# Optimization experiments

Measured on AMD Instinct MI355X. Metric: run time of the kernel, lower is better.

## Reference

```python
import jax, jax.numpy as jnp
import numpy as np

EMB_SIZE = 768
NUM_HEADS = 8


def setup_inputs() -> dict:
    key = jax.random.key(0)
    ks = jax.random.split(key, 6)
    B, N, E = 8, 1024, EMB_SIZE
    return {
        "x": jax.random.normal(ks[0], (B, N, E), dtype=jnp.float32),
        "relative_pos": jax.random.normal(ks[1], (NUM_HEADS, N, N), dtype=jnp.float32),
        "qkv_w": jax.random.normal(ks[2], (2 * E, E), dtype=jnp.float32) * 0.02,
        "qkv_b": jax.random.normal(ks[3], (2 * E,), dtype=jnp.float32) * 0.02,
        "val_w": jax.random.normal(ks[4], (E, E), dtype=jnp.float32) * 0.02,
        "val_b": jax.random.normal(ks[5], (E,), dtype=jnp.float32) * 0.02,
    }


def reference(x, relative_pos, qkv_w, qkv_b, val_w, val_b):
    B, N, E = x.shape
    H = NUM_HEADS
    D = E // H
    # qkv projection: [B, N, 2E]; last dim layout is (h, d, qk) per einops rearrange
    qkv = (x @ qkv_w.T + qkv_b).reshape(B, N, H, D, 2)
    q = jnp.transpose(qkv[..., 0], (0, 2, 1, 3))  # [B, H, N, D]
    k = jnp.transpose(qkv[..., 1], (0, 2, 1, 3))  # [B, H, N, D]
    scale = E ** 0.5  # original divides by sqrt(emb_size), not sqrt(d_head)
    energy = jnp.einsum('bhqd,bhkd->bhqk', q, k) / scale  # [B, H, N, N]
    # relative_pos [H, N, N] broadcasts over batch
    energy = jax.nn.softmax(energy + relative_pos, axis=-1)
    values = x @ val_w.T + val_b  # [B, N, E]
    return values, energy
```

## Files before the change

kernel.cpp:

```cpp
#include <hip/hip_runtime.h>
#include <hip/hip_bf16.h>

#define EMB 768
#define NH 8
#define DH 96
#define BATCH 8
#define SEQ 1024
#define M_TOT (BATCH * SEQ)
#define NCOLS (3 * EMB)

typedef float f32x4 __attribute__((ext_vector_type(4)));
typedef __bf16 bf16x8 __attribute__((ext_vector_type(8)));

__device__ __forceinline__ unsigned short f2bf_bits(float f) {
  __hip_bfloat16 b = __float2bfloat16(f);
  return *reinterpret_cast<unsigned short*>(&b);
}

__device__ __forceinline__ void gload_lds16(const void* g, void* l) {
  __builtin_amdgcn_global_load_lds(
      (__attribute__((address_space(1))) void*)(g),
      (__attribute__((address_space(3))) void*)(l), 16, 0, 0);
}

__global__ void prep_x_kernel(const float* __restrict__ x, __hip_bfloat16* __restrict__ xb) {
  const int n4 = M_TOT * EMB / 4;
  int i = blockIdx.x * blockDim.x + threadIdx.x;
  if (i < n4) {
    f32x4 v = reinterpret_cast<const f32x4*>(x)[i];
    ushort4 o;
    o.x = f2bf_bits(v[0]);
    o.y = f2bf_bits(v[1]);
    o.z = f2bf_bits(v[2]);
    o.w = f2bf_bits(v[3]);
    reinterpret_cast<ushort4*>(xb)[i] = o;
  }
}

__global__ void prep_w_kernel(const float* __restrict__ qkv_w, const float* __restrict__ qkv_b,
                              const float* __restrict__ val_w, const float* __restrict__ val_b,
                              __hip_bfloat16* __restrict__ Wall, float* __restrict__ bias) {
  const float inv_s = 0.03608439182435161f;
  int idx = blockIdx.x * 256 + threadIdx.x;
  if (idx >= NCOLS * EMB) return;
  int r = idx / EMB;
  int c = idx - r * EMB;
  float v;
  if (r < EMB) {
    int h = r / DH, d = r - h * DH;
    int src = h * 192 + 2 * d;
    v = qkv_w[(size_t)src * EMB + c] * inv_s;
    if (c == 0) bias[r] = qkv_b[src] * inv_s;
  } else if (r < 2 * EMB) {
    int r2 = r - EMB;
    int h = r2 / DH, d = r2 - h * DH;
    int src = h * 192 + 2 * d + 1;
    v = qkv_w[(size_t)src * EMB + c];
    if (c == 0) bias[r] = qkv_b[src];
  } else {
    int r3 = r - 2 * EMB;
    v = val_w[(size_t)r3 * EMB + c];
    if (c == 0) bias[r] = val_b[r3];
  }
  Wall[idx] = __float2bfloat16(v);
}

__global__ __launch_bounds__(256) void gemm_kernel(
    const __hip_bfloat16* __restrict__ xb, const __hip_bfloat16* __restrict__ Wall,
    const float* __restrict__ bias, __hip_bfloat16* __restrict__ qhead,
    __hip_bfloat16* __restrict__ khead, float* __restrict__ vout) {
  __shared__ __hip_bfloat16 As[128 * 32];
  __shared__ __hip_bfloat16 Bs[128 * 32];
  __shared__ __hip_bfloat16 Cs[128][136];
  const int tid = threadIdx.x;
  const int w = tid >> 6, l = tid & 63;
  const int m0 = blockIdx.x * 128;
  const int n0 = blockIdx.y * 128;
  const int wr = w >> 1, wc = w & 1;

  f32x4 acc[4][4] = {};

  const int sr0 = (w * 2 + 0) * 16 + (l >> 2);
  const int sr1 = (w * 2 + 1) * 16 + (l >> 2);
  const int sc = (l & 3) * 8;

  for (int kt = 0; kt < EMB / 32; ++kt) {
    const int k0 = kt * 32;
    gload_lds16(xb + (size_t)(m0 + sr0) * EMB + k0 + sc, (void*)(As + (w * 2 + 0) * 512));
    gload_lds16(xb + (size_t)(m0 + sr1) * EMB + k0 + sc, (void*)(As + (w * 2 + 1) * 512));
    gload_lds16(Wall + (size_t)(n0 + sr0) * EMB + k0 + sc, (void*)(Bs + (w * 2 + 0) * 512));
    gload_lds16(Wall + (size_t)(n0 + sr1) * EMB + k0 + sc, (void*)(Bs + (w * 2 + 1) * 512));
    __syncthreads();

    bf16x8 af[4], bfr[4];
#pragma unroll
    for (int t = 0; t < 4; ++t) {
      af[t] = *reinterpret_cast<const bf16x8*>(As + (wr * 64 + t * 16 + (l & 15)) * 32 + (l >> 4) * 8);
      bfr[t] = *reinterpret_cast<const bf16x8*>(Bs + (wc * 64 + t * 16 + (l & 15)) * 32 + (l >> 4) * 8);
    }
#pragma unroll
    for (int i = 0; i < 4; ++i)
#pragma unroll
      for (int j = 0; j < 4; ++j)
        acc[i][j] = __builtin_amdgcn_mfma_f32_16x16x32_bf16(af[i], bfr[j], acc[i][j], 0, 0, 0);
    __syncthreads();
  }

  if (n0 >= 2 * EMB) {
    const int rowbase = m0 + wr * 64;
    const int colbase = n0 - 2 * EMB + wc * 64;
#pragma unroll
    for (int j = 0; j < 4; ++j) {
      const int n = colbase + j * 16 + (l & 15);
      const float bb = bias[2 * EMB + n];
#pragma unroll
      for (int i = 0; i < 4; ++i) {
#pragma unroll
        for (int q = 0; q < 4; ++q) {
          const int m = rowbase + i * 16 + (l >> 4) * 4 + q;
          vout[(size_t)m * EMB + n] = acc[i][j][q] + bb;
        }
      }
    }
  } else {
#pragma unroll
    for (int j = 0; j < 4; ++j) {
      const int nl = wc * 64 + j * 16 + (l & 15);
      const float bb = bias[n0 + nl];
#pragma unroll
      for (int i = 0; i < 4; ++i) {
#pragma unroll
        for (int q = 0; q < 4; ++q) {
          const int ml = wr * 64 + i * 16 + (l >> 4) * 4 + q;
          Cs[ml][nl] = __float2bfloat16(acc[i][j][q] + bb);
        }
      }
    }
    __syncthreads();
    __hip_bfloat16* dst = (n0 >= EMB) ? khead : qhead;
    const int ch0 = (n0 >= EMB) ? (n0 - EMB) : n0;
    const int cg = (tid & 15) * 8;
    const int gch = ch0 + cg;
    const int hh = gch / DH, dd = gch - hh * DH;
#pragma unroll
    for (int pass = 0; pass < 8; ++pass) {
      const int r = pass * 16 + (tid >> 4);
      const int m = m0 + r;
      const int bb_ = m >> 10, mm = m & 1023;
      bf16x8 v8 = *reinterpret_cast<const bf16x8*>(&Cs[r][cg]);
      *reinterpret_cast<bf16x8*>(dst + ((size_t)(bb_ * NH + hh) * SEQ + mm) * DH + dd) = v8;
    }
  }
}

__global__ __launch_bounds__(512, 2) void attn_kernel(
    const __hip_bfloat16* __restrict__ qhead, const __hip_bfloat16* __restrict__ khead,
    const float* __restrict__ rel, float* __restrict__ eout) {
  __shared__ alignas(16) char KS[8 * 3 * 3072];
  __shared__ float redm[16][8];
  __shared__ float reds[16][8];

  const int t = threadIdx.x;
  const int w = t >> 6, l = t & 63;
  const int lr = l >> 4, lc = l & 15;
  const int flat = blockIdx.x;
  const int u = flat >> 6;
  const int b = (flat >> 3) & 7;
  const int g = u * 8 + (flat & 7);
  const int h = g >> 6;
  const int rb = g & 63;
  const int row0 = rb * 16;

  const __hip_bfloat16* qsrc = qhead + ((size_t)(b * NH + h) * SEQ + row0 + lc) * DH;
  bf16x8 qf[3];
#pragma unroll
  for (int kc = 0; kc < 3; ++kc)
    qf[kc] = *reinterpret_cast<const bf16x8*>(qsrc + kc * 32 + lr * 8);

  const float* relsrc = rel + ((size_t)h * SEQ + row0 + lc) * SEQ + w * 16 + lr * 4;
  f32x4 relv[8];
#pragma unroll
  for (int c = 0; c < 8; ++c)
    relv[c] = *reinterpret_cast<const f32x4*>(relsrc + c * 128);

  const __hip_bfloat16* ksrc =
      khead + (size_t)(b * NH + h) * SEQ * DH + (size_t)w * 16 * DH;
  char* kdst = KS + w * 9216;

#define STAGE_K(c, buf)                                                             \
  {                                                                                 \
    const __hip_bfloat16* s_ = ksrc + (size_t)(c) * 12288 + (size_t)l * 8;          \
    gload_lds16(s_, kdst + (buf) * 3072);                                           \
    gload_lds16(s_ + 512, kdst + (buf) * 3072 + 1024);                              \
    gload_lds16(s_ + 1024, kdst + (buf) * 3072 + 2048);                             \
  }

  STAGE_K(0, 0)
  STAGE_K(1, 1)

  f32x4 acc[8];
#pragma unroll
  for (int c = 0; c < 8; ++c) {
    if (c < 6) STAGE_K(c + 2, (c + 2) % 3)
    if (c < 6) {
      asm volatile("s_waitcnt vmcnt(6)" ::: "memory");
    } else if (c == 6) {
      asm volatile("s_waitcnt vmcnt(3)" ::: "memory");
    } else {
      asm volatile("s_waitcnt vmcnt(0)" ::: "memory");
    }
    __builtin_amdgcn_sched_barrier(0);
    const __hip_bfloat16* kp =
        reinterpret_cast<const __hip_bfloat16*>(kdst + (c % 3) * 3072) + lc * DH;
    f32x4 a = {0.f, 0.f, 0.f, 0.f};
    __builtin_amdgcn_s_setprio(1);
#pragma unroll
    for (int kc = 0; kc < 3; ++kc) {
      bf16x8 kf = *reinterpret_cast<const bf16x8*>(kp + kc * 32 + lr * 8);
      a = __builtin_amdgcn_mfma_f32_16x16x32_bf16(kf, qf[kc], a, 0, 0, 0);
    }
    __builtin_amdgcn_s_setprio(0);
    acc[c] = a + relv[c];
  }
#undef STAGE_K

  float mx = -3.4e38f;
#pragma unroll
  for (int c = 0; c < 8; ++c)
    mx = fmaxf(mx, fmaxf(fmaxf(acc[c][0], acc[c][1]), fmaxf(acc[c][2], acc[c][3])));
  mx = fmaxf(mx, __shfl_xor(mx, 16));
  mx = fmaxf(mx, __shfl_xor(mx, 32));
  if (l < 16) redm[lc][w] = mx;
  __syncthreads();
  float M = redm[lc][0];
#pragma unroll
  for (int i = 1; i < 8; ++i) M = fmaxf(M, redm[lc][i]);

  float sm = 0.f;
#pragma unroll
  for (int c = 0; c < 8; ++c) {
#pragma unroll
    for (int j = 0; j < 4; ++j) {
      float e = __expf(acc[c][j] - M);
      acc[c][j] = e;
      sm += e;
    }
  }
  sm += __shfl_xor(sm, 16);
  sm += __shfl_xor(sm, 32);
  if (l < 16) reds[lc][w] = sm;
  __syncthreads();
  float S = 0.f;
#pragma unroll
  for (int i = 0; i < 8; ++i) S += reds[lc][i];
  const float rinv = 1.0f / S;

  float* op = eout + ((size_t)(b * NH + h) * SEQ + row0 + lc) * SEQ + w * 16 + lr * 4;
#pragma unroll
  for (int c = 0; c < 8; ++c) {
    f32x4 v = acc[c] * rinv;
    *reinterpret_cast<f32x4*>(op + c * 128) = v;
  }
}

extern "C" void kernel_launch(void* const* d_in, const int* in_sizes, int n_in,
                              void* d_out, int out_size, void* d_ws, size_t ws_size,
                              hipStream_t stream) {
  const float* x = (const float*)d_in[0];
  const float* rel = (const float*)d_in[1];
  const float* qkv_w = (const float*)d_in[2];
  const float* qkv_b = (const float*)d_in[3];
  const float* val_w = (const float*)d_in[4];
  const float* val_b = (const float*)d_in[5];
  float* out = (float*)d_out;

  char* ws = (char*)d_ws;
  __hip_bfloat16* xb = (__hip_bfloat16*)(ws);
  __hip_bfloat16* Wall = (__hip_bfloat16*)(ws + 12582912);
  float* bias = (float*)(ws + 16121856);
  __hip_bfloat16* qhead = (__hip_bfloat16*)(ws + 16131072);
  __hip_bfloat16* khead = (__hip_bfloat16*)(ws + 28713984);

  float* vout = out;
  float* eout = out + (size_t)M_TOT * EMB;

  prep_x_kernel<<<dim3(M_TOT * EMB / 4 / 256), dim3(256), 0, stream>>>(x, xb);
  prep_w_kernel<<<dim3(NCOLS * EMB / 256), dim3(256), 0, stream>>>(qkv_w, qkv_b, val_w, val_b,
                                                                   Wall, bias);
  gemm_kernel<<<dim3(M_TOT / 128, NCOLS / 128), dim3(256), 0, stream>>>(xb, Wall, bias, qhead,
                                                                        khead, vout);
  attn_kernel<<<dim3(SEQ / 16 * NH * BATCH), dim3(512), 0, stream>>>(qhead, khead, rel, eout);
}
```

Before: 182.4 us.

## Process 32 query rows per attention block with 16 waves and swizzled K LDS

Each attention block now handles 32 query rows, split into two 16-row MFMA tiles, using 1024 threads and 16 waves. Each K tile staged into LDS is reused for both query tiles, which halves K global traffic per output row. The K staging also applies an XOR swizzle on the LDS address to avoid bank conflicts on the fragment reads. The cost is more LDS and registers per block, which may lower occupancy; the launch bounds of (1024,4) also look aggressive.

```diff
diff --git a/kernel.cpp b/kernel.cpp
--- a/kernel.cpp
+++ b/kernel.cpp
@@ -153,12 +153,12 @@
   }
 }
 
-__global__ __launch_bounds__(512, 2) void attn_kernel(
+__global__ __launch_bounds__(1024, 4) void attn_kernel(
     const __hip_bfloat16* __restrict__ qhead, const __hip_bfloat16* __restrict__ khead,
     const float* __restrict__ rel, float* __restrict__ eout) {
-  __shared__ alignas(16) char KS[8 * 3 * 3072];
-  __shared__ float redm[16][8];
-  __shared__ float reds[16][8];
+  __shared__ alignas(16) char KS[16 * 3 * 3072];
+  __shared__ float redm[32][16];
+  __shared__ float reds[32][16];
 
   const int t = threadIdx.x;
   const int w = t >> 6, l = t & 63;
@@ -167,99 +167,148 @@
   const int u = flat >> 6;
   const int b = (flat >> 3) & 7;
   const int g = u * 8 + (flat & 7);
-  const int h = g >> 6;
-  const int rb = g & 63;
-  const int row0 = rb * 16;
-
-  const __hip_bfloat16* qsrc = qhead + ((size_t)(b * NH + h) * SEQ + row0 + lc) * DH;
-  bf16x8 qf[3];
-#pragma unroll
-  for (int kc = 0; kc < 3; ++kc)
-    qf[kc] = *reinterpret_cast<const bf16x8*>(qsrc + kc * 32 + lr * 8);
-
-  const float* relsrc = rel + ((size_t)h * SEQ + row0 + lc) * SEQ + w * 16 + lr * 4;
-  f32x4 relv[8];
-#pragma unroll
-  for (int c = 0; c < 8; ++c)
-    relv[c] = *reinterpret_cast<const f32x4*>(relsrc + c * 128);
-
-  const __hip_bfloat16* ksrc =
-      khead + (size_t)(b * NH + h) * SEQ * DH + (size_t)w * 16 * DH;
+  const int h = g >> 5;
+  const int rb = g & 31;
+  const int row0 = rb * 32;
+  const size_t bh = (size_t)(b * NH + h);
+
+  const __hip_bfloat16* qbase = qhead + (bh * SEQ + row0 + lc) * DH;
+  bf16x8 qf[2][3];
+#pragma unroll
+  for (int tt = 0; tt < 2; ++tt)
+#pragma unroll
+    for (int kc = 0; kc < 3; ++kc)
+      qf[tt][kc] = *reinterpret_cast<const bf16x8*>(qbase + (size_t)(tt * 16) * DH + kc * 32 + lr * 8);
+
+  const float* relbase = rel + ((size_t)h * SEQ + row0 + lc) * SEQ + w * 16 + lr * 4;
+  f32x4 relv[4][2];
+#pragma unroll
+  for (int c = 0; c < 4; ++c)
+#pragma unroll
+    for (int tt = 0; tt < 2; ++tt)
+      relv[c][tt] = *reinterpret_cast<const f32x4*>(relbase + (size_t)(tt * 16) * SEQ + c * 256);
+
+  const __hip_bfloat16* kbh = khead + bh * SEQ * DH;
   char* kdst = KS + w * 9216;
-
-#define STAGE_K(c, buf)                                                             \
-  {                                                                                 \
-    const __hip_bfloat16* s_ = ksrc + (size_t)(c) * 12288 + (size_t)l * 8;          \
-    gload_lds16(s_, kdst + (buf) * 3072);                                           \
-    gload_lds16(s_ + 512, kdst + (buf) * 3072 + 1024);                              \
-    gload_lds16(s_ + 1024, kdst + (buf) * 3072 + 2048);                             \
+  int srcoff[3];
+#pragma unroll
+  for (int j = 0; j < 3; ++j) {
+    const int G = j * 64 + l;
+    const int r = G / 12;
+    const int slot = G - r * 12;
+    srcoff[j] = r * DH + ((slot ^ (r & 3)) << 3);
+  }
+  const int colb = w * 16;
+
+#define STAGE_K(c, buf)                                                   \
+  {                                                                       \
+    const __hip_bfloat16* s_ = kbh + (size_t)((c) * 256 + colb) * DH;     \
+    gload_lds16(s_ + srcoff[0], kdst + (buf) * 3072);                     \
+    gload_lds16(s_ + srcoff[1], kdst + (buf) * 3072 + 1024);              \
+    gload_lds16(s_ + srcoff[2], kdst + (buf) * 3072 + 2048);              \
   }
 
   STAGE_K(0, 0)
   STAGE_K(1, 1)
 
-  f32x4 acc[8];
-#pragma unroll
-  for (int c = 0; c < 8; ++c) {
-    if (c < 6) STAGE_K(c + 2, (c + 2) % 3)
-    if (c < 6) {
+  const int sw = (lc & 3) << 4;
+  const int ldsrow = lc * 192;
+  f32x4 acc[4][2];
+#pragma unroll
+  for (int c = 0; c < 4; ++c) {
+    if (c < 2) STAGE_K(c + 2, (c + 2) % 3)
+    if (c == 0 || c == 1) {
       asm volatile("s_waitcnt vmcnt(6)" ::: "memory");
-    } else if (c == 6) {
+    } else if (c == 2) {
       asm volatile("s_waitcnt vmcnt(3)" ::: "memory");
     } else {
       asm volatile("s_waitcnt vmcnt(0)" ::: "memory");
     }
     __builtin_amdgcn_sched_barrier(0);
-    const __hip_bfloat16* kp =
-        reinterpret_cast<const __hip_bfloat16*>(kdst + (c % 3) * 3072) + lc * DH;
-    f32x4 a = {0.f, 0.f, 0.f, 0.f};
+    const char* kp = kdst + (c % 3) * 3072 + ldsrow;
+    bf16x8 kf[3];
+#pragma unroll
+    for (int kc = 0; kc < 3; ++kc)
+      kf[kc] = *reinterpret_cast<const bf16x8*>(kp + ((kc * 64 + lr * 16) ^ sw));
     __builtin_amdgcn_s_setprio(1);
 #pragma unroll
-    for (int kc = 0; kc < 3; ++kc) {
-      bf16x8 kf = *reinterpret_cast<const bf16x8*>(kp + kc * 32 + lr * 8);
-      a = __builtin_amdgcn_mfma_f32_16x16x32_bf16(kf, qf[kc], a, 0, 0, 0);
+    for (int tt = 0; tt < 2; ++tt) {
+      f32x4 a = {0.f, 0.f, 0.f, 0.f};
+#pragma unroll
+      for (int kc = 0; kc < 3; ++kc)
+        a = __builtin_amdgcn_mfma_f32_16x16x32_bf16(kf[kc], qf[tt][kc], a, 0, 0, 0);
+      acc[c][tt] = a + relv[c][tt];
     }
     __builtin_amdgcn_s_setprio(0);
-    acc[c] = a + relv[c];
   }
 #undef STAGE_K
 
-  float mx = -3.4e38f;
-#pragma unroll
-  for (int c = 0; c < 8; ++c)
-    mx = fmaxf(mx, fmaxf(fmaxf(acc[c][0], acc[c][1]), fmaxf(acc[c][2], acc[c][3])));
-  mx = fmaxf(mx, __shfl_xor(mx, 16));
-  mx = fmaxf(mx, __shfl_xor(mx, 32));
-  if (l < 16) redm[lc][w] = mx;
+  float mx[2] = {-3.4e38f, -3.4e38f};
+#pragma unroll
+  for (int c = 0; c < 4; ++c)
+#pragma unroll
+    for (int tt = 0; tt < 2; ++tt)
+      mx[tt] = fmaxf(mx[tt],
+                     fmaxf(fmaxf(acc[c][tt][0], acc[c][tt][1]),
+                           fmaxf(acc[c][tt][2], acc[c][tt][3])));
+#pragma unroll
+  for (int tt = 0; tt < 2; ++tt) {
+    mx[tt] = fmaxf(mx[tt], __shfl_xor(mx[tt], 16));
+    mx[tt] = fmaxf(mx[tt], __shfl_xor(mx[tt], 32));
+  }
+  if (l < 16) {
+    redm[lc][w] = mx[0];
+    redm[16 + lc][w] = mx[1];
+  }
   __syncthreads();
-  float M = redm[lc][0];
-#pragma unroll
-  for (int i = 1; i < 8; ++i) M = fmaxf(M, redm[lc][i]);
-
-  float sm = 0.f;
-#pragma unroll
-  for (int c = 0; c < 8; ++c) {
-#pragma unroll
-    for (int j = 0; j < 4; ++j) {
-      float e = __expf(acc[c][j] - M);
-      acc[c][j] = e;
-      sm += e;
-    }
-  }
-  sm += __shfl_xor(sm, 16);
-  sm += __shfl_xor(sm, 32);
-  if (l < 16) reds[lc][w] = sm;
+  float M[2];
+#pragma unroll
+  for (int tt = 0; tt < 2; ++tt) {
+    const f32x4* rm = reinterpret_cast<const f32x4*>(redm[tt * 16 + lc]);
+    f32x4 m4 = rm[0];
+    m4 = __builtin_elementwise_max(m4, rm[1]);
+    m4 = __builtin_elementwise_max(m4, rm[2]);
+    m4 = __builtin_elementwise_max(m4, rm[3]);
+    M[tt] = fmaxf(fmaxf(m4[0], m4[1]), fmaxf(m4[2], m4[3]));
+  }
+
+  float sm[2] = {0.f, 0.f};
+#pragma unroll
+  for (int c = 0; c < 4; ++c)
+#pragma unroll
+    for (int tt = 0; tt < 2; ++tt)
+#pragma unroll
+      for (int j = 0; j < 4; ++j) {
+        float e = __expf(acc[c][tt][j] - M[tt]);
+        acc[c][tt][j] = e;
+        sm[tt] += e;
+      }
+#pragma unroll
+  for (int tt = 0; tt < 2; ++tt) {
+    sm[tt] += __shfl_xor(sm[tt], 16);
+    sm[tt] += __shfl_xor(sm[tt], 32);
+  }
+  if (l < 16) {
+    reds[lc][w] = sm[0];
+    reds[16 + lc][w] = sm[1];
+  }
   __syncthreads();
-  float S = 0.f;
-#pragma unroll
-  for (int i = 0; i < 8; ++i) S += reds[lc][i];
-  const float rinv = 1.0f / S;
-
-  float* op = eout + ((size_t)(b * NH + h) * SEQ + row0 + lc) * SEQ + w * 16 + lr * 4;
-#pragma unroll
-  for (int c = 0; c < 8; ++c) {
-    f32x4 v = acc[c] * rinv;
-    *reinterpret_cast<f32x4*>(op + c * 128) = v;
+  float rinv[2];
+#pragma unroll
+  for (int tt = 0; tt < 2; ++tt) {
+    const f32x4* rs = reinterpret_cast<const f32x4*>(reds[tt * 16 + lc]);
+    f32x4 s4 = rs[0] + rs[1] + rs[2] + rs[3];
+    rinv[tt] = 1.0f / (s4[0] + s4[1] + s4[2] + s4[3]);
+  }
+
+#pragma unroll
+  for (int tt = 0; tt < 2; ++tt) {
+    float* op = eout + ((bh * SEQ) + row0 + tt * 16 + lc) * SEQ + w * 16 + lr * 4;
+#pragma unroll
+    for (int c = 0; c < 4; ++c) {
+      f32x4 v = acc[c][tt] * rinv[tt];
+      *reinterpret_cast<f32x4*>(op + c * 256) = v;
+    }
   }
 }
 
@@ -289,5 +338,5 @@
                                                                    Wall, bias);
   gemm_kernel<<<dim3(M_TOT / 128, NCOLS / 128), dim3(256), 0, stream>>>(xb, Wall, bias, qhead,
                                                                         khead, vout);
-  attn_kernel<<<dim3(SEQ / 16 * NH * BATCH), dim3(512), 0, stream>>>(qhead, khead, rel, eout);
-}
+  attn_kernel<<<dim3(SEQ / 32 * NH * BATCH), dim3(1024), 0, stream>>>(qhead, khead, rel, eout);
+}
```

Result: slower. 196.2 us (+7.6%).

## Make attention blocks persistent over four row tiles with cross-tile prefetch

Applied to the files above, without the earlier changes.

Each attention block now handles four consecutive 16-row tiles instead of one, and the grid shrinks by four. While computing the current tile, it prefetches the next tile's K chunks, Q fragments and relative-position values, so loads overlap with compute. The K staging buffer drops from triple to double buffering, which cuts LDS use, and launch bounds rise to allow more blocks per CU. Barriers become raw s_barrier calls with explicit waitcnts. The risks are fragile vmcnt accounting, more register pressure, and fewer blocks to balance across CUs.

```diff
diff --git a/kernel.cpp b/kernel.cpp
--- a/kernel.cpp
+++ b/kernel.cpp
@@ -153,10 +153,10 @@
   }
 }
 
-__global__ __launch_bounds__(512, 2) void attn_kernel(
+__global__ __launch_bounds__(512, 4) void attn_kernel(
     const __hip_bfloat16* __restrict__ qhead, const __hip_bfloat16* __restrict__ khead,
     const float* __restrict__ rel, float* __restrict__ eout) {
-  __shared__ alignas(16) char KS[8 * 3 * 3072];
+  __shared__ alignas(16) char KS[8 * 2 * 3072];
   __shared__ float redm[16][8];
   __shared__ float reds[16][8];
 
@@ -164,103 +164,143 @@
   const int w = t >> 6, l = t & 63;
   const int lr = l >> 4, lc = l & 15;
   const int flat = blockIdx.x;
-  const int u = flat >> 6;
+  const int v = flat >> 6;
   const int b = (flat >> 3) & 7;
-  const int g = u * 8 + (flat & 7);
-  const int h = g >> 6;
-  const int rb = g & 63;
-  const int row0 = rb * 16;
-
-  const __hip_bfloat16* qsrc = qhead + ((size_t)(b * NH + h) * SEQ + row0 + lc) * DH;
-  bf16x8 qf[3];
+  const int g = v * 8 + (flat & 7);
+  const int h = g >> 4;
+  const int rg = g & 15;
+  const size_t bh = (size_t)(b * NH + h);
+
+  const __hip_bfloat16* kbh = khead + bh * SEQ * DH;
+  char* kdst = KS + w * 6144;
+
+#define STAGE_K(k, buf)                                                            \
+  {                                                                                \
+    const __hip_bfloat16* s_ = kbh + (size_t)((k) * 128 + w * 16) * DH + l * 8;    \
+    gload_lds16(s_, kdst + (buf) * 3072);                                          \
+    gload_lds16(s_ + 512, kdst + (buf) * 3072 + 1024);                             \
+    gload_lds16(s_ + 1024, kdst + (buf) * 3072 + 2048);                            \
+  }
+
+  bf16x8 qfc[3], qfn[3];
+  f32x4 relv[8], acc[8];
+
+  const __hip_bfloat16* qsrc0 = qhead + (bh * SEQ + rg * 64 + lc) * DH;
 #pragma unroll
   for (int kc = 0; kc < 3; ++kc)
-    qf[kc] = *reinterpret_cast<const bf16x8*>(qsrc + kc * 32 + lr * 8);
-
-  const float* relsrc = rel + ((size_t)h * SEQ + row0 + lc) * SEQ + w * 16 + lr * 4;
-  f32x4 relv[8];
-#pragma unroll
-  for (int c = 0; c < 8; ++c)
-    relv[c] = *reinterpret_cast<const f32x4*>(relsrc + c * 128);
-
-  const __hip_bfloat16* ksrc =
-      khead + (size_t)(b * NH + h) * SEQ * DH + (size_t)w * 16 * DH;
-  char* kdst = KS + w * 9216;
-
-#define STAGE_K(c, buf)                                                             \
-  {                                                                                 \
-    const __hip_bfloat16* s_ = ksrc + (size_t)(c) * 12288 + (size_t)l * 8;          \
-    gload_lds16(s_, kdst + (buf) * 3072);                                           \
-    gload_lds16(s_ + 512, kdst + (buf) * 3072 + 1024);                              \
-    gload_lds16(s_ + 1024, kdst + (buf) * 3072 + 2048);                             \
-  }
-
+    qfc[kc] = *reinterpret_cast<const bf16x8*>(qsrc0 + kc * 32 + lr * 8);
+  const float* relbase = rel + ((size_t)h * SEQ + rg * 64 + lc) * SEQ + w * 16 + lr * 4;
+#pragma unroll
+  for (int k = 0; k < 8; ++k)
+    relv[k] = *reinterpret_cast<const f32x4*>(relbase + k * 128);
   STAGE_K(0, 0)
   STAGE_K(1, 1)
 
-  f32x4 acc[8];
-#pragma unroll
-  for (int c = 0; c < 8; ++c) {
-    if (c < 6) STAGE_K(c + 2, (c + 2) % 3)
-    if (c < 6) {
-      asm volatile("s_waitcnt vmcnt(6)" ::: "memory");
-    } else if (c == 6) {
-      asm volatile("s_waitcnt vmcnt(3)" ::: "memory");
-    } else {
-      asm volatile("s_waitcnt vmcnt(0)" ::: "memory");
-    }
-    __builtin_amdgcn_sched_barrier(0);
-    const __hip_bfloat16* kp =
-        reinterpret_cast<const __hip_bfloat16*>(kdst + (c % 3) * 3072) + lc * DH;
-    f32x4 a = {0.f, 0.f, 0.f, 0.f};
-    __builtin_amdgcn_s_setprio(1);
-#pragma unroll
-    for (int kc = 0; kc < 3; ++kc) {
-      bf16x8 kf = *reinterpret_cast<const bf16x8*>(kp + kc * 32 + lr * 8);
-      a = __builtin_amdgcn_mfma_f32_16x16x32_bf16(kf, qf[kc], a, 0, 0, 0);
-    }
-    __builtin_amdgcn_s_setprio(0);
-    acc[c] = a + relv[c];
+  for (int item = 0; item < 4; ++item) {
+    const int row0 = rg * 64 + item * 16;
+#pragma unroll
+    for (int k = 0; k < 8; ++k) {
+      if (k == 0) {
+        if (item == 0) { asm volatile("s_waitcnt vmcnt(3)" ::: "memory"); }
+        else           { asm volatile("s_waitcnt vmcnt(22)" ::: "memory"); }
+      } else if (k == 1) {
+        if (item == 0) { asm volatile("s_waitcnt vmcnt(3)" ::: "memory"); }
+        else           { asm volatile("s_waitcnt vmcnt(11)" ::: "memory"); }
+      } else if (k == 7) {
+        if (item == 3) { asm volatile("s_waitcnt vmcnt(0)" ::: "memory"); }
+        else           { asm volatile("s_waitcnt vmcnt(6)" ::: "memory"); }
+      } else {
+        asm volatile("s_waitcnt vmcnt(3)" ::: "memory");
+      }
+      __builtin_amdgcn_sched_barrier(0);
+
+      const char* kp = kdst + (k & 1) * 3072 + lc * 192;
+      bf16x8 kf[3];
+#pragma unroll
+      for (int kc = 0; kc < 3; ++kc)
+        kf[kc] = *reinterpret_cast<const bf16x8*>(kp + kc * 64 + lr * 16);
+      asm volatile("s_waitcnt lgkmcnt(0)" ::: "memory");
+      __builtin_amdgcn_sched_barrier(0);
+
+      if (k <= 5) {
+        STAGE_K(k + 2, k & 1)
+      } else if (k == 6) {
+        if (item < 3) {
+          STAGE_K(0, 0)
+          __builtin_amdgcn_sched_barrier(0);
+          const __hip_bfloat16* qn = qhead + (bh * SEQ + row0 + 16 + lc) * DH;
+#pragma unroll
+          for (int kc = 0; kc < 3; ++kc)
+            qfn[kc] = *reinterpret_cast<const bf16x8*>(qn + kc * 32 + lr * 8);
+        }
+      } else {
+        if (item < 3) STAGE_K(1, 1)
+      }
+
+      __builtin_amdgcn_s_setprio(1);
+      f32x4 a = {0.f, 0.f, 0.f, 0.f};
+#pragma unroll
+      for (int kc = 0; kc < 3; ++kc)
+        a = __builtin_amdgcn_mfma_f32_16x16x32_bf16(kf[kc], qfc[kc], a, 0, 0, 0);
+      __builtin_amdgcn_s_setprio(0);
+      acc[k] = a + relv[k];
+
+      if (k == 7 && item < 3) {
+        const float* rn = relbase + (size_t)(item + 1) * 16 * SEQ;
+#pragma unroll
+        for (int kk = 0; kk < 8; ++kk)
+          relv[kk] = *reinterpret_cast<const f32x4*>(rn + kk * 128);
+      }
+    }
+
+    float mx = -3.4e38f;
+#pragma unroll
+    for (int k = 0; k < 8; ++k)
+      mx = fmaxf(mx, fmaxf(fmaxf(acc[k][0], acc[k][1]), fmaxf(acc[k][2], acc[k][3])));
+    mx = fmaxf(mx, __shfl_xor(mx, 16));
+    mx = fmaxf(mx, __shfl_xor(mx, 32));
+    if (l < 16) redm[lc][w] = mx;
+    asm volatile("s_waitcnt lgkmcnt(0)" ::: "memory");
+    __builtin_amdgcn_s_barrier();
+    asm volatile("" ::: "memory");
+    float M = redm[lc][0];
+#pragma unroll
+    for (int i = 1; i < 8; ++i) M = fmaxf(M, redm[lc][i]);
+
+    float sm = 0.f;
+#pragma unroll
+    for (int k = 0; k < 8; ++k) {
+#pragma unroll
+      for (int j = 0; j < 4; ++j) {
+        float e = __expf(acc[k][j] - M);
+        acc[k][j] = e;
+        sm += e;
+      }
+    }
+    sm += __shfl_xor(sm, 16);
+    sm += __shfl_xor(sm, 32);
+    if (l < 16) reds[lc][w] = sm;
+    asm volatile("s_waitcnt lgkmcnt(0)" ::: "memory");
+    __builtin_amdgcn_s_barrier();
+    asm volatile("" ::: "memory");
+    float S = 0.f;
+#pragma unroll
+    for (int i = 0; i < 8; ++i) S += reds[lc][i];
+    const float rinv = 1.0f / S;
+
+    float* op = eout + (bh * SEQ + row0 + lc) * SEQ + w * 16 + lr * 4;
+#pragma unroll
+    for (int k = 0; k < 8; ++k) {
+      f32x4 vv = acc[k] * rinv;
+      *reinterpret_cast<f32x4*>(op + k * 128) = vv;
+    }
+
+    if (item < 3) {
+#pragma unroll
+      for (int kc = 0; kc < 3; ++kc) qfc[kc] = qfn[kc];
+    }
   }
 #undef STAGE_K
-
-  float mx = -3.4e38f;
-#pragma unroll
-  for (int c = 0; c < 8; ++c)
-    mx = fmaxf(mx, fmaxf(fmaxf(acc[c][0], acc[c][1]), fmaxf(acc[c][2], acc[c][3])));
-  mx = fmaxf(mx, __shfl_xor(mx, 16));
-  mx = fmaxf(mx, __shfl_xor(mx, 32));
-  if (l < 16) redm[lc][w] = mx;
-  __syncthreads();
-  float M = redm[lc][0];
-#pragma unroll
-  for (int i = 1; i < 8; ++i) M = fmaxf(M, redm[lc][i]);
-
-  float sm = 0.f;
-#pragma unroll
-  for (int c = 0; c < 8; ++c) {
-#pragma unroll
-    for (int j = 0; j < 4; ++j) {
-      float e = __expf(acc[c][j] - M);
-      acc[c][j] = e;
-      sm += e;
-    }
-  }
-  sm += __shfl_xor(sm, 16);
-  sm += __shfl_xor(sm, 32);
-  if (l < 16) reds[lc][w] = sm;
-  __syncthreads();
-  float S = 0.f;
-#pragma unroll
-  for (int i = 0; i < 8; ++i) S += reds[lc][i];
-  const float rinv = 1.0f / S;
-
-  float* op = eout + ((size_t)(b * NH + h) * SEQ + row0 + lc) * SEQ + w * 16 + lr * 4;
-#pragma unroll
-  for (int c = 0; c < 8; ++c) {
-    f32x4 v = acc[c] * rinv;
-    *reinterpret_cast<f32x4*>(op + c * 128) = v;
-  }
 }
 
 extern "C" void kernel_launch(void* const* d_in, const int* in_sizes, int n_in,
@@ -289,5 +329,5 @@
                                                                    Wall, bias);
   gemm_kernel<<<dim3(M_TOT / 128, NCOLS / 128), dim3(256), 0, stream>>>(xb, Wall, bias, qhead,
                                                                         khead, vout);
-  attn_kernel<<<dim3(SEQ / 16 * NH * BATCH), dim3(512), 0, stream>>>(qhead, khead, rel, eout);
-}
+  attn_kernel<<<dim3(SEQ / 64 * NH * BATCH), dim3(512), 0, stream>>>(qhead, khead, rel, eout);
+}
```

Result: slower. 266.0 us (+45.8%).

## Give each wave a contiguous 128-key slice and use nontemporal energy stores

Applied to the files above, without the earlier changes.

Changes how key columns are split across the eight waves. Before, each wave handled 16-key chunks strided by 128; now each wave owns one contiguous block of 128 keys, so the K staging, relative-position reads and energy writes all touch contiguous memory per wave. The energy output stores also switch to nontemporal stores so the large write-once output does not pollute the cache. Contiguous per-wave spans may give better DRAM and cache locality, and the per-row 64-byte segments from different waves still cover the whole row.

```diff
diff --git a/kernel.cpp b/kernel.cpp
--- a/kernel.cpp
+++ b/kernel.cpp
@@ -170,26 +170,26 @@
   const int h = g >> 6;
   const int rb = g & 63;
   const int row0 = rb * 16;
-
-  const __hip_bfloat16* qsrc = qhead + ((size_t)(b * NH + h) * SEQ + row0 + lc) * DH;
+  const size_t bh = (size_t)(b * NH + h);
+
+  const __hip_bfloat16* qsrc = qhead + (bh * SEQ + row0 + lc) * DH;
   bf16x8 qf[3];
 #pragma unroll
   for (int kc = 0; kc < 3; ++kc)
     qf[kc] = *reinterpret_cast<const bf16x8*>(qsrc + kc * 32 + lr * 8);
 
-  const float* relsrc = rel + ((size_t)h * SEQ + row0 + lc) * SEQ + w * 16 + lr * 4;
+  const float* relsrc = rel + ((size_t)h * SEQ + row0 + lc) * SEQ + w * 128 + lr * 4;
   f32x4 relv[8];
 #pragma unroll
-  for (int c = 0; c < 8; ++c)
-    relv[c] = *reinterpret_cast<const f32x4*>(relsrc + c * 128);
-
-  const __hip_bfloat16* ksrc =
-      khead + (size_t)(b * NH + h) * SEQ * DH + (size_t)w * 16 * DH;
+  for (int s = 0; s < 8; ++s)
+    relv[s] = *reinterpret_cast<const f32x4*>(relsrc + s * 16);
+
+  const __hip_bfloat16* ksrc = khead + bh * SEQ * DH + (size_t)w * 128 * DH;
   char* kdst = KS + w * 9216;
 
-#define STAGE_K(c, buf)                                                             \
+#define STAGE_K(s, buf)                                                             \
   {                                                                                 \
-    const __hip_bfloat16* s_ = ksrc + (size_t)(c) * 12288 + (size_t)l * 8;          \
+    const __hip_bfloat16* s_ = ksrc + (size_t)(s) * 1536 + (size_t)l * 8;           \
     gload_lds16(s_, kdst + (buf) * 3072);                                           \
     gload_lds16(s_ + 512, kdst + (buf) * 3072 + 1024);                              \
     gload_lds16(s_ + 1024, kdst + (buf) * 3072 + 2048);                             \
@@ -200,18 +200,18 @@
 
   f32x4 acc[8];
 #pragma unroll
-  for (int c = 0; c < 8; ++c) {
-    if (c < 6) STAGE_K(c + 2, (c + 2) % 3)
-    if (c < 6) {
+  for (int s = 0; s < 8; ++s) {
+    if (s < 6) STAGE_K(s + 2, (s + 2) % 3)
+    if (s < 6) {
       asm volatile("s_waitcnt vmcnt(6)" ::: "memory");
-    } else if (c == 6) {
+    } else if (s == 6) {
       asm volatile("s_waitcnt vmcnt(3)" ::: "memory");
     } else {
       asm volatile("s_waitcnt vmcnt(0)" ::: "memory");
     }
     __builtin_amdgcn_sched_barrier(0);
     const __hip_bfloat16* kp =
-        reinterpret_cast<const __hip_bfloat16*>(kdst + (c % 3) * 3072) + lc * DH;
+        reinterpret_cast<const __hip_bfloat16*>(kdst + (s % 3) * 3072) + lc * DH;
     f32x4 a = {0.f, 0.f, 0.f, 0.f};
     __builtin_amdgcn_s_setprio(1);
 #pragma unroll
@@ -220,14 +220,14 @@
       a = __builtin_amdgcn_mfma_f32_16x16x32_bf16(kf, qf[kc], a, 0, 0, 0);
     }
     __builtin_amdgcn_s_setprio(0);
-    acc[c] = a + relv[c];
+    acc[s] = a + relv[s];
   }
 #undef STAGE_K
 
   float mx = -3.4e38f;
 #pragma unroll
-  for (int c = 0; c < 8; ++c)
-    mx = fmaxf(mx, fmaxf(fmaxf(acc[c][0], acc[c][1]), fmaxf(acc[c][2], acc[c][3])));
+  for (int s = 0; s < 8; ++s)
+    mx = fmaxf(mx, fmaxf(fmaxf(acc[s][0], acc[s][1]), fmaxf(acc[s][2], acc[s][3])));
   mx = fmaxf(mx, __shfl_xor(mx, 16));
   mx = fmaxf(mx, __shfl_xor(mx, 32));
   if (l < 16) redm[lc][w] = mx;
@@ -238,11 +238,11 @@
 
   float sm = 0.f;
 #pragma unroll
-  for (int c = 0; c < 8; ++c) {
+  for (int s = 0; s < 8; ++s) {
 #pragma unroll
     for (int j = 0; j < 4; ++j) {
-      float e = __expf(acc[c][j] - M);
-      acc[c][j] = e;
+      float e = __expf(acc[s][j] - M);
+      acc[s][j] = e;
       sm += e;
     }
   }
@@ -255,11 +255,11 @@
   for (int i = 0; i < 8; ++i) S += reds[lc][i];
   const float rinv = 1.0f / S;
 
-  float* op = eout + ((size_t)(b * NH + h) * SEQ + row0 + lc) * SEQ + w * 16 + lr * 4;
-#pragma unroll
-  for (int c = 0; c < 8; ++c) {
-    f32x4 v = acc[c] * rinv;
-    *reinterpret_cast<f32x4*>(op + c * 128) = v;
+  float* op = eout + (bh * SEQ + row0 + lc) * SEQ + w * 128 + lr * 4;
+#pragma unroll
+  for (int s = 0; s < 8; ++s) {
+    f32x4 v = acc[s] * rinv;
+    __builtin_nontemporal_store(v, reinterpret_cast<f32x4*>(op + s * 16));
   }
 }
 
```

New measurement: 161.1 us. -11.7%, faster.
